# Performance work log

Measured on AMD Instinct MI355X. Metric: run time of the kernel, lower is better.

The kernel has to match this reference:

```python
import jax, jax.numpy as jnp
import numpy as np
from jax import lax

B, T, BYTE_LEN, EMB = 8, 4096, 8, 64
FILTERS = [(1, 4), (2, 8), (3, 12), (4, 16), (5, 20), (6, 24), (7, 28)]
LAST_DIM = sum(c for _, c in FILTERS)  # 112
OUT_DIM = 512


def setup_inputs() -> dict:
    key = jax.random.key(0)
    ks = jax.random.split(key, 32)
    inp = {"features": jax.random.normal(ks[0], (B, T, BYTE_LEN, EMB), dtype=jnp.float32)}
    for i, (w, c) in enumerate(FILTERS):
        inp[f"conv_w{i+1}"] = jax.random.normal(ks[1 + i], (c, EMB, w), dtype=jnp.float32) * 0.05
        inp[f"conv_b{i+1}"] = jax.random.normal(ks[8 + i], (c,), dtype=jnp.float32) * 0.05
    inp["hw_w1"] = jax.random.normal(ks[15], (2 * LAST_DIM, LAST_DIM), dtype=jnp.float32) * 0.05
    inp["hw_b1"] = jnp.concatenate([jnp.zeros(LAST_DIM), jnp.ones(LAST_DIM)]).astype(jnp.float32)
    inp["hw_w2"] = jax.random.normal(ks[16], (2 * LAST_DIM, LAST_DIM), dtype=jnp.float32) * 0.05
    inp["hw_b2"] = jnp.concatenate([jnp.zeros(LAST_DIM), jnp.ones(LAST_DIM)]).astype(jnp.float32)
    inp["proj_w"] = jax.random.normal(ks[17], (OUT_DIM, LAST_DIM), dtype=jnp.float32) * 0.05
    inp["proj_b"] = jax.random.normal(ks[18], (OUT_DIM,), dtype=jnp.float32) * 0.05
    return inp


def _conv_branch(x, w, b):
    # x: [N, EMB, BYTE_LEN], w: [out_c, EMB, width] -> max over time, relu -> [N, out_c]
    y = lax.conv_general_dilated(x, w, window_strides=(1,), padding='VALID',
                                 dimension_numbers=('NCH', 'OIH', 'NCH'))
    y = y + b[None, :, None]
    return jax.nn.relu(jnp.max(y, axis=-1))


def _highway_layer(x, w, b):
    p = x @ w.T + b
    proj_x, gate = jnp.split(p, 2, axis=-1)
    g = jax.nn.sigmoid(gate)
    return g * x + (1.0 - g) * jax.nn.relu(proj_x)


def reference(features, conv_w1, conv_w2, conv_w3, conv_w4, conv_w5, conv_w6, conv_w7,
              conv_b1, conv_b2, conv_b3, conv_b4, conv_b5, conv_b6, conv_b7,
              hw_w1, hw_b1, hw_w2, hw_b2, proj_w, proj_b):
    b, t, byte_len, emb = features.shape
    # transpose(2,3).view(-1, emb, byte_len)
    x = features.transpose(0, 1, 3, 2).reshape(-1, emb, byte_len)  # [B*T, EMB, BYTE_LEN]
    ws = [conv_w1, conv_w2, conv_w3, conv_w4, conv_w5, conv_w6, conv_w7]
    bs = [conv_b1, conv_b2, conv_b3, conv_b4, conv_b5, conv_b6, conv_b7]
    branches = [_conv_branch(x, w, bb) for w, bb in zip(ws, bs)]
    h = jnp.concatenate(branches, axis=-1)  # [B*T, LAST_DIM]
    h = _highway_layer(h, hw_w1, hw_b1)
    h = _highway_layer(h, hw_w2, hw_b2)
    out = h @ proj_w.T + proj_b  # [B*T, OUT_DIM]
    return out.reshape(b, t, -1)
```

## Files before the change

kernel.cpp:

```cpp
#include <hip/hip_runtime.h>

typedef __attribute__((ext_vector_type(8))) short short8;
typedef __attribute__((ext_vector_type(4))) float f32x4;

#define KDIM 512
#define NCT  30
#define BCHUNK 32768

__device__ __forceinline__ unsigned short f2bf(float x) {
    unsigned u = __float_as_uint(x);
    return (unsigned short)((u + 0x7FFFu + ((u >> 16) & 1u)) >> 16);
}
__device__ __forceinline__ float bf2f(unsigned short h) {
    return __uint_as_float(((unsigned)h) << 16);
}

__device__ __forceinline__ void stage16(const void* g, void* l, int lane) {
    __builtin_amdgcn_global_load_lds(
        (const __attribute__((address_space(1))) unsigned int*)g,
        (__attribute__((address_space(3))) unsigned int*)l, 16, 0, 0);
}

__global__ void prep_kernel(const float* __restrict__ w1, const float* __restrict__ w2,
                            const float* __restrict__ w3, const float* __restrict__ w4,
                            const float* __restrict__ w5, const float* __restrict__ w6,
                            const float* __restrict__ w7, const float* __restrict__ hw1,
                            const float* __restrict__ hw2, const float* __restrict__ pw,
                            unsigned short* __restrict__ WC, unsigned short* __restrict__ W1s,
                            unsigned short* __restrict__ W2s, unsigned short* __restrict__ Ps) {
    int gid = blockIdx.x * 256 + threadIdx.x;
    if (gid < 245760) {
        int k = gid / 480, col = gid % 480;
        const float* wp; int cbnd, NP, C, W;
        if (col < 32)       { wp = w1; cbnd = 0;   NP = 8; C = 4;  W = 1; }
        else if (col < 96)  { wp = w2; cbnd = 32;  NP = 7; C = 8;  W = 2; }
        else if (col < 176) { wp = w3; cbnd = 96;  NP = 6; C = 12; W = 3; }
        else if (col < 256) { wp = w4; cbnd = 176; NP = 5; C = 16; W = 4; }
        else if (col < 336) { wp = w5; cbnd = 256; NP = 4; C = 20; W = 5; }
        else if (col < 416) { wp = w6; cbnd = 336; NP = 3; C = 24; W = 6; }
        else                { wp = w7; cbnd = 416; NP = 2; C = 28; W = 7; }
        int c2 = col - cbnd, oc = c2 / NP, p = c2 - oc * NP;
        int j = k >> 6, e = k & 63, dk = j - p;
        float v = 0.f;
        if (oc < C && dk >= 0 && dk < W) v = wp[(oc * 64 + e) * W + dk];
        int q = k >> 5, kr = k & 31;
        WC[q * 16384 + ((col >> 4) * 64 + ((kr >> 3) * 16 + (col & 15))) * 8 + (kr & 7)] = f2bf(v);
    } else if (gid < 245760 + 57344) {
        int x = gid - 245760;
        const float* src = (x < 28672) ? hw1 : hw2;
        unsigned short* dst = (x < 28672) ? W1s : W2s;
        if (x >= 28672) x -= 28672;
        int k = x / 224, n = x % 224;
        float v = (k < 112) ? src[n * 112 + k] : 0.f;
        int q = k >> 5, kr = k & 31;
        dst[q * 8192 + ((n >> 4) * 64 + ((kr >> 3) * 16 + (n & 15))) * 8 + (kr & 7)] = f2bf(v);
    } else if (gid < 245760 + 57344 + 65536) {
        int x = gid - 303104;
        int k = x / 512, n = x % 512;
        float v = (k < 112) ? pw[n * 112 + k] : 0.f;
        int q = k >> 5, kr = k & 31;
        Ps[((q * 32 + (n >> 4)) * 64 + ((kr >> 3) * 16 + (n & 15))) * 8 + (kr & 7)] = f2bf(v);
    }
}

template <int T0, int NT>
__device__ __forceinline__ void dump_phase(float* Cb, const f32x4* acc, int wave, int lane) {
    int r0 = wave * 16 + ((lane >> 4) * 4);
    int c0 = lane & 15;
#pragma unroll
    for (int tt = 0; tt < NT; ++tt)
#pragma unroll
        for (int r = 0; r < 4; ++r)
            Cb[(r0 + r) * 161 + tt * 16 + c0] = acc[T0 + tt][r];
}

__device__ void reduce_phase(const float* Cb, unsigned short* ht, int tid,
                             int cA, int NPA, int choffA, int colbA, const float* cbA,
                             int cB, int NPB, int choffB, int colbB, const float* cbB) {
    int noc = cA + cB;
    for (int idx = tid; idx < 64 * noc; idx += 256) {
        int row = idx & 63, ocp = idx >> 6;
        bool isB = ocp >= cA;
        int oc = isB ? ocp - cA : ocp;
        int NP = isB ? NPB : NPA;
        int colb = isB ? colbB : colbA;
        int choff = isB ? choffB : choffA;
        const float* cb = isB ? cbB : cbA;
        const float* src = Cb + row * 161 + colb + oc * NP;
        float m = src[0];
        for (int k = 1; k < NP; ++k) m = fmaxf(m, src[k]);
        float v = fmaxf(m + cb[oc], 0.f);
        ht[row * 136 + choff + oc] = f2bf(v);
    }
}

__global__ __launch_bounds__(256, 2) void fused_kernel(
        const float* __restrict__ feat, const unsigned short* __restrict__ WC,
        const float* cb0, const float* cb1, const float* cb2, const float* cb3,
        const float* cb4, const float* cb5, const float* cb6,
        const unsigned short* __restrict__ W1, const unsigned short* __restrict__ W2,
        const unsigned short* __restrict__ PW,
        const float* __restrict__ hb1, const float* __restrict__ hb2,
        const float* __restrict__ pb, float* __restrict__ out) {
    __shared__ __align__(16) char sm[65536];
    const int tid = threadIdx.x, lane = tid & 63, wave = tid >> 6;
    const int c0 = lane & 15, kq = lane >> 4;
    const int m0 = blockIdx.x * 64;
    f32x4 zero = {0.f, 0.f, 0.f, 0.f};

    const float* arow = feat + (size_t)(m0 + wave * 16 + c0) * KDIM + kq * 8;
    short8 af[16];
#pragma unroll
    for (int q = 0; q < 16; ++q) {
        float t[8];
        *(float4*)(t)     = *(const float4*)(arow + q * 32);
        *(float4*)(t + 4) = *(const float4*)(arow + q * 32 + 4);
        short8 v;
#pragma unroll
        for (int i = 0; i < 8; ++i) v[i] = (short)f2bf(t[i]);
        af[q] = v;
    }

    f32x4 acc[NCT];
#pragma unroll
    for (int t = 0; t < NCT; ++t) acc[t] = zero;

    for (int i = tid; i < 2048; i += 256)
        stage16(WC + i * 8, sm + (i - lane) * 16, lane);

#pragma unroll
    for (int q = 0; q < 16; ++q) {
        if (q < 15) {
            const unsigned short* src = WC + (q + 1) * 16384;
            char* dst = sm + ((q + 1) & 1) * BCHUNK;
            for (int i = tid; i < 2048; i += 256)
                stage16(src + i * 8, dst + (i - lane) * 16, lane);
            asm volatile("s_waitcnt vmcnt(8)" ::: "memory");
        } else {
            asm volatile("s_waitcnt vmcnt(0)" ::: "memory");
        }
        __builtin_amdgcn_s_barrier();
        const char* bb = sm + (q & 1) * BCHUNK;
        __builtin_amdgcn_s_setprio(1);
#pragma unroll
        for (int t = 0; t < NCT; ++t) {
            short8 b = *(const short8*)(bb + (t * 64 + lane) * 16);
            acc[t] = __builtin_amdgcn_mfma_f32_16x16x32_bf16(af[q], b, acc[t], 0, 0, 0);
        }
        __builtin_amdgcn_s_setprio(0);
        asm volatile("s_waitcnt lgkmcnt(0)" ::: "memory");
        __builtin_amdgcn_s_barrier();
    }

    float* Cb = (float*)sm;
    unsigned short* ht = (unsigned short*)(sm + 41216);
    __syncthreads();
    for (int i = tid; i < 1024; i += 256)
        ht[(i >> 4) * 136 + 112 + (i & 15)] = 0;
    dump_phase<0, 6>(Cb, acc, wave, lane);
    __syncthreads();
    reduce_phase(Cb, ht, tid, 4, 8, 0, 0, cb0, 8, 7, 4, 32, cb1);
    __syncthreads();
    dump_phase<6, 10>(Cb, acc, wave, lane);
    __syncthreads();
    reduce_phase(Cb, ht, tid, 12, 6, 12, 0, cb2, 16, 5, 24, 80, cb3);
    __syncthreads();
    dump_phase<16, 10>(Cb, acc, wave, lane);
    __syncthreads();
    reduce_phase(Cb, ht, tid, 20, 4, 40, 0, cb4, 24, 3, 60, 80, cb5);
    __syncthreads();
    dump_phase<26, 4>(Cb, acc, wave, lane);
    __syncthreads();
    reduce_phase(Cb, ht, tid, 28, 2, 84, 0, cb6, 0, 1, 0, 0, cb6);
    __syncthreads();

    char* wb = sm;
    short8 a2[4];
#pragma unroll
    for (int q = 0; q < 4; ++q)
        a2[q] = *(const short8*)((const char*)ht + (wave * 16 + c0) * 272 + q * 64 + kq * 16);
    for (int i = tid; i < 1024; i += 256)
        stage16(W1 + i * 8, wb + (i - lane) * 16, lane);

    f32x4 acc2[14];
#pragma unroll
    for (int t = 0; t < 14; ++t) acc2[t] = zero;
#pragma unroll
    for (int q = 0; q < 4; ++q) {
        if (q < 3) {
            const unsigned short* src = W1 + (q + 1) * 8192;
            char* dst = wb + ((q + 1) & 1) * 16384;
            for (int i = tid; i < 1024; i += 256)
                stage16(src + i * 8, dst + (i - lane) * 16, lane);
        } else {
            for (int i = tid; i < 1024; i += 256)
                stage16(W2 + i * 8, wb + (i - lane) * 16, lane);
        }
        asm volatile("s_waitcnt vmcnt(4)" ::: "memory");
        __builtin_amdgcn_s_barrier();
        const char* bb = wb + (q & 1) * 16384;
#pragma unroll
        for (int t = 0; t < 14; ++t) {
            short8 b = *(const short8*)(bb + (t * 64 + lane) * 16);
            acc2[t] = __builtin_amdgcn_mfma_f32_16x16x32_bf16(a2[q], b, acc2[t], 0, 0, 0);
        }
        asm volatile("s_waitcnt lgkmcnt(0)" ::: "memory");
        __builtin_amdgcn_s_barrier();
    }

#pragma unroll
    for (int t = 0; t < 7; ++t) {
        float bp = hb1[t * 16 + c0], bg = hb1[112 + t * 16 + c0];
#pragma unroll
        for (int r = 0; r < 4; ++r) {
            int row = wave * 16 + kq * 4 + r;
            int col = t * 16 + c0;
            float px = acc2[t][r] + bp;
            float gt = acc2[t + 7][r] + bg;
            float g = 1.f / (1.f + __expf(-gt));
            float hres = bf2f(ht[row * 136 + col]);
            ht[row * 136 + col] = f2bf(g * hres + (1.f - g) * fmaxf(px, 0.f));
        }
    }

    short8 a3[4];
#pragma unroll
    for (int q = 0; q < 4; ++q)
        a3[q] = *(const short8*)((const char*)ht + (wave * 16 + c0) * 272 + q * 64 + kq * 16);

    f32x4 acc3[14];
#pragma unroll
    for (int t = 0; t < 14; ++t) acc3[t] = zero;
#pragma unroll
    for (int q = 0; q < 4; ++q) {
        if (q < 3) {
            const unsigned short* src = W2 + (q + 1) * 8192;
            char* dst = wb + ((q + 1) & 1) * 16384;
            for (int i = tid; i < 1024; i += 256)
                stage16(src + i * 8, dst + (i - lane) * 16, lane);
        } else {
            for (int i = tid; i < 1024; i += 256)
                stage16(PW + i * 8, wb + (i - lane) * 16, lane);
        }
        asm volatile("s_waitcnt vmcnt(4)" ::: "memory");
        __builtin_amdgcn_s_barrier();
        const char* bb = wb + (q & 1) * 16384;
#pragma unroll
        for (int t = 0; t < 14; ++t) {
            short8 b = *(const short8*)(bb + (t * 64 + lane) * 16);
            acc3[t] = __builtin_amdgcn_mfma_f32_16x16x32_bf16(a3[q], b, acc3[t], 0, 0, 0);
        }
        asm volatile("s_waitcnt lgkmcnt(0)" ::: "memory");
        __builtin_amdgcn_s_barrier();
    }

#pragma unroll
    for (int t = 0; t < 7; ++t) {
        float bp = hb2[t * 16 + c0], bg = hb2[112 + t * 16 + c0];
#pragma unroll
        for (int r = 0; r < 4; ++r) {
            int row = wave * 16 + kq * 4 + r;
            int col = t * 16 + c0;
            float px = acc3[t][r] + bp;
            float gt = acc3[t + 7][r] + bg;
            float g = 1.f / (1.f + __expf(-gt));
            float hres = bf2f(ht[row * 136 + col]);
            ht[row * 136 + col] = f2bf(g * hres + (1.f - g) * fmaxf(px, 0.f));
        }
    }

    short8 a4[4];
#pragma unroll
    for (int q = 0; q < 4; ++q)
        a4[q] = *(const short8*)((const char*)ht + (wave * 16 + c0) * 272 + q * 64 + kq * 16);

    char* pwb = sm;
    f32x4 acc4[32];
#pragma unroll
    for (int t = 0; t < 32; ++t) acc4[t] = zero;
#pragma unroll
    for (int c = 0; c < 8; ++c) {
        if (c < 7) {
            const unsigned short* src = PW + (c + 1) * 8192;
            char* dst = pwb + ((c + 1) & 1) * 16384;
            for (int i = tid; i < 1024; i += 256)
                stage16(src + i * 8, dst + (i - lane) * 16, lane);
            asm volatile("s_waitcnt vmcnt(4)" ::: "memory");
        } else {
            asm volatile("s_waitcnt vmcnt(0)" ::: "memory");
        }
        __builtin_amdgcn_s_barrier();
        const char* bb = pwb + (c & 1) * 16384;
        __builtin_amdgcn_s_setprio(1);
#pragma unroll
        for (int tt = 0; tt < 16; ++tt) {
            short8 b = *(const short8*)(bb + (tt * 64 + lane) * 16);
            acc4[(c & 1) * 16 + tt] =
                __builtin_amdgcn_mfma_f32_16x16x32_bf16(a4[c >> 1], b, acc4[(c & 1) * 16 + tt], 0, 0, 0);
        }
        __builtin_amdgcn_s_setprio(0);
        asm volatile("s_waitcnt lgkmcnt(0)" ::: "memory");
        __builtin_amdgcn_s_barrier();
    }

    float* ot = (float*)sm;
#pragma unroll
    for (int half = 0; half < 2; ++half) {
        __syncthreads();
#pragma unroll
        for (int t16 = 0; t16 < 16; ++t16) {
            int col = (half * 16 + t16) * 16 + c0;
            float b = pb[col];
#pragma unroll
            for (int r = 0; r < 4; ++r)
                ot[(wave * 16 + kq * 4 + r) * 256 + t16 * 16 + c0] = acc4[half * 16 + t16][r] + b;
        }
        __syncthreads();
        for (int i = tid; i < 4096; i += 256) {
            int row = i >> 6, c = i & 63;
            *(float4*)(out + (size_t)(m0 + row) * 512 + half * 256 + c * 4) = ((const float4*)ot)[i];
        }
    }
}

extern "C" void kernel_launch(void* const* d_in, const int* in_sizes, int n_in,
                              void* d_out, int out_size, void* d_ws, size_t ws_size,
                              hipStream_t stream) {
    const float* feat = (const float*)d_in[0];
    const float* cw[7];
    const float* cb[7];
    for (int f = 0; f < 7; ++f) {
        cw[f] = (const float*)d_in[1 + 2 * f];
        cb[f] = (const float*)d_in[2 + 2 * f];
    }
    const float* hw_w1 = (const float*)d_in[15];
    const float* hw_b1 = (const float*)d_in[16];
    const float* hw_w2 = (const float*)d_in[17];
    const float* hw_b2 = (const float*)d_in[18];
    const float* pw    = (const float*)d_in[19];
    const float* pb    = (const float*)d_in[20];
    float* out = (float*)d_out;

    char* ws = (char*)d_ws;
    unsigned short* WC  = (unsigned short*)ws;
    unsigned short* W1s = (unsigned short*)(ws + 524288);
    unsigned short* W2s = (unsigned short*)(ws + 589824);
    unsigned short* Ps  = (unsigned short*)(ws + 655360);

    prep_kernel<<<1440, 256, 0, stream>>>(cw[0], cw[1], cw[2], cw[3], cw[4], cw[5], cw[6],
                                          hw_w1, hw_w2, pw, WC, W1s, W2s, Ps);
    fused_kernel<<<512, 256, 0, stream>>>(feat, WC, cb[0], cb[1], cb[2], cb[3], cb[4], cb[5], cb[6],
                                          W1s, W2s, Ps, hw_b1, hw_b2, pb, out);
}
```

Before: 192.1 us.

## Double block rows to 128 with 512 threads sharing staged weight tiles

Each block now covers 128 rows with 8 waves instead of 64 rows with 4 waves, so every staged conv/highway/projection weight chunk in LDS is reused by twice as many rows, halving global weight traffic per row. The highway and projection weights are repacked into smaller 8KB chunks and streamed through a 3-slot ring buffer, and the conv epilogue is split into more dump/reduce phases with tighter LDS strides to fit 128 rows. Grid shrinks to 256 blocks and setprio hints are dropped; risks include higher register pressure at 512 threads with launch bounds 2, fewer blocks than CUs, and more barriers in the epilogue.

```diff
diff --git a/kernel.cpp b/kernel.cpp
--- a/kernel.cpp
+++ b/kernel.cpp
@@ -5,7 +5,10 @@
 
 #define KDIM 512
 #define NCT  30
-#define BCHUNK 32768
+#define CB_STRIDE 97
+#define HT_OFF    28672
+#define HT_STRIDE 132
+#define RING_CH   8192
 
 __device__ __forceinline__ unsigned short f2bf(float x) {
     unsigned u = __float_as_uint(x);
@@ -53,32 +56,36 @@
         int k = x / 224, n = x % 224;
         float v = (k < 112) ? src[n * 112 + k] : 0.f;
         int q = k >> 5, kr = k & 31;
-        dst[q * 8192 + ((n >> 4) * 64 + ((kr >> 3) * 16 + (n & 15))) * 8 + (kr & 7)] = f2bf(v);
+        int h = (n >= 112) ? 1 : 0;
+        int tt = (n >> 4) - h * 7;
+        dst[(q * 2 + h) * 4096 + (tt * 64 + ((kr >> 3) * 16 + (n & 15))) * 8 + (kr & 7)] = f2bf(v);
     } else if (gid < 245760 + 57344 + 65536) {
         int x = gid - 303104;
         int k = x / 512, n = x % 512;
         float v = (k < 112) ? pw[n * 112 + k] : 0.f;
         int q = k >> 5, kr = k & 31;
-        Ps[((q * 32 + (n >> 4)) * 64 + ((kr >> 3) * 16 + (n & 15))) * 8 + (kr & 7)] = f2bf(v);
+        int c = q * 4 + (n >> 7);
+        int tt = (n >> 4) & 7;
+        Ps[c * 4096 + (tt * 64 + ((kr >> 3) * 16 + (n & 15))) * 8 + (kr & 7)] = f2bf(v);
     }
 }
 
 template <int T0, int NT>
-__device__ __forceinline__ void dump_phase(float* Cb, const f32x4* acc, int wave, int lane) {
-    int r0 = wave * 16 + ((lane >> 4) * 4);
+__device__ __forceinline__ void dump_phase(float* Cb, const f32x4* acc, int w4, int lane) {
+    int r0 = w4 * 16 + ((lane >> 4) * 4);
     int c0 = lane & 15;
 #pragma unroll
     for (int tt = 0; tt < NT; ++tt)
 #pragma unroll
         for (int r = 0; r < 4; ++r)
-            Cb[(r0 + r) * 161 + tt * 16 + c0] = acc[T0 + tt][r];
+            Cb[(r0 + r) * CB_STRIDE + tt * 16 + c0] = acc[T0 + tt][r];
 }
 
 __device__ void reduce_phase(const float* Cb, unsigned short* ht, int tid,
                              int cA, int NPA, int choffA, int colbA, const float* cbA,
                              int cB, int NPB, int choffB, int colbB, const float* cbB) {
     int noc = cA + cB;
-    for (int idx = tid; idx < 64 * noc; idx += 256) {
+    for (int idx = tid; idx < 64 * noc; idx += 512) {
         int row = idx & 63, ocp = idx >> 6;
         bool isB = ocp >= cA;
         int oc = isB ? ocp - cA : ocp;
@@ -86,15 +93,29 @@
         int colb = isB ? colbB : colbA;
         int choff = isB ? choffB : choffA;
         const float* cb = isB ? cbB : cbA;
-        const float* src = Cb + row * 161 + colb + oc * NP;
+        const float* src = Cb + row * CB_STRIDE + colb + oc * NP;
         float m = src[0];
         for (int k = 1; k < NP; ++k) m = fmaxf(m, src[k]);
         float v = fmaxf(m + cb[oc], 0.f);
-        ht[row * 136 + choff + oc] = f2bf(v);
-    }
-}
-
-__global__ __launch_bounds__(256, 2) void fused_kernel(
+        ht[row * HT_STRIDE + choff + oc] = f2bf(v);
+    }
+}
+
+template <int T0, int NT>
+__device__ __forceinline__ void epi_phase(float* Cb, unsigned short* ht, const f32x4* acc,
+                                          int tid, int wave, int lane,
+                                          int cA, int NPA, int choffA, int colbA, const float* cbA,
+                                          int cB, int NPB, int choffB, int colbB, const float* cbB) {
+    for (int g = 0; g < 2; ++g) {
+        if ((wave >> 2) == g) dump_phase<T0, NT>(Cb, acc, wave & 3, lane);
+        __syncthreads();
+        reduce_phase(Cb, ht + g * 64 * HT_STRIDE, tid,
+                     cA, NPA, choffA, colbA, cbA, cB, NPB, choffB, colbB, cbB);
+        __syncthreads();
+    }
+}
+
+__global__ __launch_bounds__(512, 2) void fused_kernel(
         const float* __restrict__ feat, const unsigned short* __restrict__ WC,
         const float* cb0, const float* cb1, const float* cb2, const float* cb3,
         const float* cb4, const float* cb5, const float* cb6,
@@ -105,7 +126,7 @@
     __shared__ __align__(16) char sm[65536];
     const int tid = threadIdx.x, lane = tid & 63, wave = tid >> 6;
     const int c0 = lane & 15, kq = lane >> 4;
-    const int m0 = blockIdx.x * 64;
+    const int m0 = blockIdx.x * 128;
     f32x4 zero = {0.f, 0.f, 0.f, 0.f};
 
     const float* arow = feat + (size_t)(m0 + wave * 16 + c0) * KDIM + kq * 8;
@@ -125,130 +146,118 @@
 #pragma unroll
     for (int t = 0; t < NCT; ++t) acc[t] = zero;
 
-    for (int i = tid; i < 2048; i += 256)
+    for (int i = tid; i < 2048; i += 512)
         stage16(WC + i * 8, sm + (i - lane) * 16, lane);
 
 #pragma unroll
     for (int q = 0; q < 16; ++q) {
         if (q < 15) {
             const unsigned short* src = WC + (q + 1) * 16384;
-            char* dst = sm + ((q + 1) & 1) * BCHUNK;
-            for (int i = tid; i < 2048; i += 256)
+            char* dst = sm + ((q + 1) & 1) * 32768;
+            for (int i = tid; i < 2048; i += 512)
                 stage16(src + i * 8, dst + (i - lane) * 16, lane);
-            asm volatile("s_waitcnt vmcnt(8)" ::: "memory");
+            asm volatile("s_waitcnt vmcnt(4)" ::: "memory");
         } else {
             asm volatile("s_waitcnt vmcnt(0)" ::: "memory");
         }
         __builtin_amdgcn_s_barrier();
-        const char* bb = sm + (q & 1) * BCHUNK;
-        __builtin_amdgcn_s_setprio(1);
+        const char* bb = sm + (q & 1) * 32768;
 #pragma unroll
         for (int t = 0; t < NCT; ++t) {
             short8 b = *(const short8*)(bb + (t * 64 + lane) * 16);
             acc[t] = __builtin_amdgcn_mfma_f32_16x16x32_bf16(af[q], b, acc[t], 0, 0, 0);
         }
-        __builtin_amdgcn_s_setprio(0);
         asm volatile("s_waitcnt lgkmcnt(0)" ::: "memory");
         __builtin_amdgcn_s_barrier();
     }
 
     float* Cb = (float*)sm;
-    unsigned short* ht = (unsigned short*)(sm + 41216);
+    unsigned short* ht = (unsigned short*)(sm + HT_OFF);
+    for (int i = tid; i < 2048; i += 512)
+        ht[(i >> 4) * HT_STRIDE + 112 + (i & 15)] = 0;
     __syncthreads();
-    for (int i = tid; i < 1024; i += 256)
-        ht[(i >> 4) * 136 + 112 + (i & 15)] = 0;
-    dump_phase<0, 6>(Cb, acc, wave, lane);
-    __syncthreads();
-    reduce_phase(Cb, ht, tid, 4, 8, 0, 0, cb0, 8, 7, 4, 32, cb1);
-    __syncthreads();
-    dump_phase<6, 10>(Cb, acc, wave, lane);
-    __syncthreads();
-    reduce_phase(Cb, ht, tid, 12, 6, 12, 0, cb2, 16, 5, 24, 80, cb3);
-    __syncthreads();
-    dump_phase<16, 10>(Cb, acc, wave, lane);
-    __syncthreads();
-    reduce_phase(Cb, ht, tid, 20, 4, 40, 0, cb4, 24, 3, 60, 80, cb5);
-    __syncthreads();
-    dump_phase<26, 4>(Cb, acc, wave, lane);
-    __syncthreads();
-    reduce_phase(Cb, ht, tid, 28, 2, 84, 0, cb6, 0, 1, 0, 0, cb6);
-    __syncthreads();
-
-    char* wb = sm;
+    epi_phase<0, 6>(Cb, ht, acc, tid, wave, lane, 4, 8, 0, 0, cb0, 8, 7, 4, 32, cb1);
+    epi_phase<6, 5>(Cb, ht, acc, tid, wave, lane, 12, 6, 12, 0, cb2, 0, 1, 0, 0, cb2);
+    epi_phase<11, 5>(Cb, ht, acc, tid, wave, lane, 16, 5, 24, 0, cb3, 0, 1, 0, 0, cb3);
+    epi_phase<16, 5>(Cb, ht, acc, tid, wave, lane, 20, 4, 40, 0, cb4, 0, 1, 0, 0, cb4);
+    epi_phase<21, 5>(Cb, ht, acc, tid, wave, lane, 24, 3, 60, 0, cb5, 0, 1, 0, 0, cb5);
+    epi_phase<26, 4>(Cb, ht, acc, tid, wave, lane, 28, 2, 84, 0, cb6, 0, 1, 0, 0, cb6);
+
+    char* ring = sm;
     short8 a2[4];
 #pragma unroll
     for (int q = 0; q < 4; ++q)
-        a2[q] = *(const short8*)((const char*)ht + (wave * 16 + c0) * 272 + q * 64 + kq * 16);
-    for (int i = tid; i < 1024; i += 256)
-        stage16(W1 + i * 8, wb + (i - lane) * 16, lane);
+        a2[q] = *(const short8*)((const char*)ht + (wave * 16 + c0) * 264 + q * 64 + kq * 16);
+
+    stage16(W1 + tid * 8, ring + (tid - lane) * 16, lane);
+    stage16(W1 + 4096 + tid * 8, ring + RING_CH + (tid - lane) * 16, lane);
 
     f32x4 acc2[14];
 #pragma unroll
     for (int t = 0; t < 14; ++t) acc2[t] = zero;
 #pragma unroll
-    for (int q = 0; q < 4; ++q) {
-        if (q < 3) {
-            const unsigned short* src = W1 + (q + 1) * 8192;
-            char* dst = wb + ((q + 1) & 1) * 16384;
-            for (int i = tid; i < 1024; i += 256)
-                stage16(src + i * 8, dst + (i - lane) * 16, lane);
-        } else {
-            for (int i = tid; i < 1024; i += 256)
-                stage16(W2 + i * 8, wb + (i - lane) * 16, lane);
-        }
-        asm volatile("s_waitcnt vmcnt(4)" ::: "memory");
-        __builtin_amdgcn_s_barrier();
-        const char* bb = wb + (q & 1) * 16384;
-#pragma unroll
-        for (int t = 0; t < 14; ++t) {
-            short8 b = *(const short8*)(bb + (t * 64 + lane) * 16);
-            acc2[t] = __builtin_amdgcn_mfma_f32_16x16x32_bf16(a2[q], b, acc2[t], 0, 0, 0);
+    for (int i = 0; i < 8; ++i) {
+        {
+            const unsigned short* src = (i < 6) ? (W1 + (i + 2) * 4096) : (W2 + (i - 6) * 4096);
+            char* dst = ring + ((i + 2) % 3) * RING_CH;
+            stage16(src + tid * 8, dst + (tid - lane) * 16, lane);
+        }
+        asm volatile("s_waitcnt vmcnt(2)" ::: "memory");
+        __builtin_amdgcn_s_barrier();
+        const char* bb = ring + (i % 3) * RING_CH;
+        const int q = i >> 1, h = i & 1;
+#pragma unroll
+        for (int tt = 0; tt < 7; ++tt) {
+            short8 b = *(const short8*)(bb + (tt * 64 + lane) * 16);
+            acc2[h * 7 + tt] = __builtin_amdgcn_mfma_f32_16x16x32_bf16(a2[q], b, acc2[h * 7 + tt], 0, 0, 0);
         }
         asm volatile("s_waitcnt lgkmcnt(0)" ::: "memory");
         __builtin_amdgcn_s_barrier();
     }
 
 #pragma unroll
-    for (int t = 0; t < 7; ++t) {
+    for (int t = 0; t < 14; ++t) {
         float bp = hb1[t * 16 + c0], bg = hb1[112 + t * 16 + c0];
+        (void)bg;
 #pragma unroll
         for (int r = 0; r < 4; ++r) {
             int row = wave * 16 + kq * 4 + r;
             int col = t * 16 + c0;
-            float px = acc2[t][r] + bp;
-            float gt = acc2[t + 7][r] + bg;
-            float g = 1.f / (1.f + __expf(-gt));
-            float hres = bf2f(ht[row * 136 + col]);
-            ht[row * 136 + col] = f2bf(g * hres + (1.f - g) * fmaxf(px, 0.f));
-        }
-    }
+            if (t < 7) {
+                float px = acc2[t][r] + bp;
+                float gt = acc2[t + 7][r] + hb1[112 + t * 16 + c0];
+                float g = 1.f / (1.f + __expf(-gt));
+                float hres = bf2f(ht[row * HT_STRIDE + col]);
+                ht[row * HT_STRIDE + col] = f2bf(g * hres + (1.f - g) * fmaxf(px, 0.f));
+            }
+        }
+    }
+    asm volatile("s_waitcnt lgkmcnt(0)" ::: "memory");
+    __builtin_amdgcn_s_barrier();
 
     short8 a3[4];
 #pragma unroll
     for (int q = 0; q < 4; ++q)
-        a3[q] = *(const short8*)((const char*)ht + (wave * 16 + c0) * 272 + q * 64 + kq * 16);
+        a3[q] = *(const short8*)((const char*)ht + (wave * 16 + c0) * 264 + q * 64 + kq * 16);
 
     f32x4 acc3[14];
 #pragma unroll
     for (int t = 0; t < 14; ++t) acc3[t] = zero;
 #pragma unroll
-    for (int q = 0; q < 4; ++q) {
-        if (q < 3) {
-            const unsigned short* src = W2 + (q + 1) * 8192;
-            char* dst = wb + ((q + 1) & 1) * 16384;
-            for (int i = tid; i < 1024; i += 256)
-                stage16(src + i * 8, dst + (i - lane) * 16, lane);
-        } else {
-            for (int i = tid; i < 1024; i += 256)
-                stage16(PW + i * 8, wb + (i - lane) * 16, lane);
-        }
-        asm volatile("s_waitcnt vmcnt(4)" ::: "memory");
-        __builtin_amdgcn_s_barrier();
-        const char* bb = wb + (q & 1) * 16384;
-#pragma unroll
-        for (int t = 0; t < 14; ++t) {
-            short8 b = *(const short8*)(bb + (t * 64 + lane) * 16);
-            acc3[t] = __builtin_amdgcn_mfma_f32_16x16x32_bf16(a3[q], b, acc3[t], 0, 0, 0);
+    for (int j = 0; j < 8; ++j) {
+        {
+            const unsigned short* src = (j < 6) ? (W2 + (j + 2) * 4096) : (PW + (j - 6) * 4096);
+            char* dst = ring + ((j + 10) % 3) * RING_CH;
+            stage16(src + tid * 8, dst + (tid - lane) * 16, lane);
+        }
+        asm volatile("s_waitcnt vmcnt(2)" ::: "memory");
+        __builtin_amdgcn_s_barrier();
+        const char* bb = ring + ((j + 8) % 3) * RING_CH;
+        const int q = j >> 1, h = j & 1;
+#pragma unroll
+        for (int tt = 0; tt < 7; ++tt) {
+            short8 b = *(const short8*)(bb + (tt * 64 + lane) * 16);
+            acc3[h * 7 + tt] = __builtin_amdgcn_mfma_f32_16x16x32_bf16(a3[q], b, acc3[h * 7 + tt], 0, 0, 0);
         }
         asm volatile("s_waitcnt lgkmcnt(0)" ::: "memory");
         __builtin_amdgcn_s_barrier();
@@ -264,61 +273,61 @@
             float px = acc3[t][r] + bp;
             float gt = acc3[t + 7][r] + bg;
             float g = 1.f / (1.f + __expf(-gt));
-            float hres = bf2f(ht[row * 136 + col]);
-            ht[row * 136 + col] = f2bf(g * hres + (1.f - g) * fmaxf(px, 0.f));
-        }
-    }
+            float hres = bf2f(ht[row * HT_STRIDE + col]);
+            ht[row * HT_STRIDE + col] = f2bf(g * hres + (1.f - g) * fmaxf(px, 0.f));
+        }
+    }
+    asm volatile("s_waitcnt lgkmcnt(0)" ::: "memory");
+    __builtin_amdgcn_s_barrier();
 
     short8 a4[4];
 #pragma unroll
     for (int q = 0; q < 4; ++q)
-        a4[q] = *(const short8*)((const char*)ht + (wave * 16 + c0) * 272 + q * 64 + kq * 16);
-
-    char* pwb = sm;
+        a4[q] = *(const short8*)((const char*)ht + (wave * 16 + c0) * 264 + q * 64 + kq * 16);
+
     f32x4 acc4[32];
 #pragma unroll
     for (int t = 0; t < 32; ++t) acc4[t] = zero;
 #pragma unroll
-    for (int c = 0; c < 8; ++c) {
-        if (c < 7) {
-            const unsigned short* src = PW + (c + 1) * 8192;
-            char* dst = pwb + ((c + 1) & 1) * 16384;
-            for (int i = tid; i < 1024; i += 256)
-                stage16(src + i * 8, dst + (i - lane) * 16, lane);
-            asm volatile("s_waitcnt vmcnt(4)" ::: "memory");
+    for (int k = 0; k < 16; ++k) {
+        if (k < 14) {
+            const unsigned short* src = PW + (k + 2) * 4096;
+            char* dst = ring + ((k + 18) % 3) * RING_CH;
+            stage16(src + tid * 8, dst + (tid - lane) * 16, lane);
+            asm volatile("s_waitcnt vmcnt(2)" ::: "memory");
+        } else if (k == 14) {
+            asm volatile("s_waitcnt vmcnt(1)" ::: "memory");
         } else {
             asm volatile("s_waitcnt vmcnt(0)" ::: "memory");
         }
         __builtin_amdgcn_s_barrier();
-        const char* bb = pwb + (c & 1) * 16384;
-        __builtin_amdgcn_s_setprio(1);
-#pragma unroll
-        for (int tt = 0; tt < 16; ++tt) {
+        const char* bb = ring + ((k + 16) % 3) * RING_CH;
+        const int q = k >> 2, e = k & 3;
+#pragma unroll
+        for (int tt = 0; tt < 8; ++tt) {
             short8 b = *(const short8*)(bb + (tt * 64 + lane) * 16);
-            acc4[(c & 1) * 16 + tt] =
-                __builtin_amdgcn_mfma_f32_16x16x32_bf16(a4[c >> 1], b, acc4[(c & 1) * 16 + tt], 0, 0, 0);
-        }
-        __builtin_amdgcn_s_setprio(0);
+            acc4[e * 8 + tt] = __builtin_amdgcn_mfma_f32_16x16x32_bf16(a4[q], b, acc4[e * 8 + tt], 0, 0, 0);
+        }
         asm volatile("s_waitcnt lgkmcnt(0)" ::: "memory");
         __builtin_amdgcn_s_barrier();
     }
 
     float* ot = (float*)sm;
 #pragma unroll
-    for (int half = 0; half < 2; ++half) {
+    for (int e = 0; e < 4; ++e) {
         __syncthreads();
 #pragma unroll
-        for (int t16 = 0; t16 < 16; ++t16) {
-            int col = (half * 16 + t16) * 16 + c0;
+        for (int tt = 0; tt < 8; ++tt) {
+            int col = e * 128 + tt * 16 + c0;
             float b = pb[col];
 #pragma unroll
             for (int r = 0; r < 4; ++r)
-                ot[(wave * 16 + kq * 4 + r) * 256 + t16 * 16 + c0] = acc4[half * 16 + t16][r] + b;
+                ot[(wave * 16 + kq * 4 + r) * 128 + tt * 16 + c0] = acc4[e * 8 + tt][r] + b;
         }
         __syncthreads();
-        for (int i = tid; i < 4096; i += 256) {
-            int row = i >> 6, c = i & 63;
-            *(float4*)(out + (size_t)(m0 + row) * 512 + half * 256 + c * 4) = ((const float4*)ot)[i];
+        for (int i = tid; i < 4096; i += 512) {
+            int row = i >> 5, c = i & 31;
+            *(float4*)(out + (size_t)(m0 + row) * 512 + e * 128 + c * 4) = ((const float4*)ot)[i];
         }
     }
 }
@@ -349,6 +358,6 @@
 
     prep_kernel<<<1440, 256, 0, stream>>>(cw[0], cw[1], cw[2], cw[3], cw[4], cw[5], cw[6],
                                           hw_w1, hw_w2, pw, WC, W1s, W2s, Ps);
-    fused_kernel<<<512, 256, 0, stream>>>(feat, WC, cb[0], cb[1], cb[2], cb[3], cb[4], cb[5], cb[6],
+    fused_kernel<<<256, 512, 0, stream>>>(feat, WC, cb[0], cb[1], cb[2], cb[3], cb[4], cb[5], cb[6],
                                           W1s, W2s, Ps, hw_b1, hw_b2, pb, out);
 }
```

Result: no change. 191.7 us (-0.2%).
